# Performance work log

Measured on AMD Instinct MI355X. Metric: run time of the kernel, lower is better.

The kernel has to match this reference:

```python
import jax, jax.numpy as jnp
import numpy as np
from jax import lax
from itertools import combinations

# ---- static MiniRocket config (mirrors MiniRocketFeatures defaults) ----
NUM_KERNELS = 84
KSIZE = 9
C_IN = 9
SEQ_LEN = 2048
BATCH = 64
NUM_FEATURES = 10000
MAX_DIL_PER_KERNEL = 32

def _set_dilations(input_length):
    nfpk = NUM_FEATURES // NUM_KERNELS          # 119 features per kernel
    tmd = min(nfpk, MAX_DIL_PER_KERNEL)         # 32
    multiplier = nfpk / tmd
    max_exponent = np.log2((input_length - 1) / (KSIZE - 1))
    dilations, counts = np.unique(
        np.logspace(0, max_exponent, tmd, base=2).astype(np.int32),
        return_counts=True)
    nfd = (counts * multiplier).astype(np.int32)
    remainder = nfpk - nfd.sum()
    i = 0
    while remainder > 0:
        nfd[i] += 1; remainder -= 1; i = (i + 1) % len(nfd)
    return [int(d) for d in dilations], [int(n) for n in nfd]

DILATIONS, NFD = _set_dilations(SEQ_LEN)
NUM_DIL = len(DILATIONS)
PADDINGS = [(KSIZE - 1) * d // 2 for d in DILATIONS]
MAX_NF = max(NFD)


def _make_kernels():
    # 84 fixed ternary kernels: -1 everywhere, 2 at each 3-of-9 combination
    idx = np.array(list(combinations(range(KSIZE), 3)))       # [84, 3]
    k = -np.ones((NUM_KERNELS, KSIZE), np.float32)
    k[np.arange(NUM_KERNELS)[:, None], idx] = 2.0
    # grouped conv weight: repeat the 84-kernel block per input channel
    return np.tile(k, (C_IN, 1)).reshape(C_IN * NUM_KERNELS, 1, KSIZE)


def setup_inputs() -> dict:
    key = jax.random.key(0)
    k1, k2, k3 = jax.random.split(key, 3)
    x = jax.random.normal(k1, (BATCH, C_IN, SEQ_LEN), dtype=jnp.float32)
    kernels = jnp.asarray(_make_kernels())                    # [c_in*84, 1, 9]
    # per-dilation 0/1 channel-combination masks (1, c_in, 84, 1) stacked
    channel_combinations = jax.random.bernoulli(
        k2, 0.5, (NUM_DIL, C_IN, NUM_KERNELS)).astype(jnp.float32)
    # per-dilation biases [84, nf_i], padded to MAX_NF for stacking
    biases = jax.random.normal(
        k3, (NUM_DIL, NUM_KERNELS, MAX_NF), dtype=jnp.float32)
    return {"x": x, "kernels": kernels,
            "channel_combinations": channel_combinations, "biases": biases}


def _ppv(C, bias):
    # C: [B, K, T], bias: [K, nf] -> proportion of values above bias, [B, K*nf]
    ppv = (C[..., None] > bias[None, :, None, :]).astype(jnp.float32).mean(2)
    return ppv.reshape(C.shape[0], -1)


def reference(x, kernels, channel_combinations, biases):
    B = x.shape[0]
    feats = []
    for i, (dilation, padding) in enumerate(zip(DILATIONS, PADDINGS)):
        pad1 = i % 2
        # grouped dilated conv: [B, c_in*84, L] (output length == L since p = 4d)
        C = lax.conv_general_dilated(
            x, kernels, window_strides=(1,), padding=[(padding, padding)],
            rhs_dilation=(dilation,), feature_group_count=C_IN,
            dimension_numbers=("NCH", "OIH", "NCH"))
        C = C.reshape(B, C_IN, NUM_KERNELS, -1)
        # channel combine: multiply by 0/1 mask, sum over channels -> [B, 84, L]
        C = (C * channel_combinations[i][None, :, :, None]).sum(1)
        bias = biases[i][:, :NFD[i]]                          # [84, nf_i]
        # even-index kernels use full (padded) output
        feats.append(_ppv(C[:, pad1::2], bias[pad1::2]))
        # odd-index kernels use the valid (un-padded) region
        feats.append(_ppv(C[:, 1 - pad1::2, padding:-padding],
                          bias[1 - pad1::2]))
    return jnp.concatenate(feats, axis=1)                     # [B, 9996]
```

## Files before the change

### kernel.cpp

```cpp
#include <hip/hip_runtime.h>

#define NKER 84
#define NCH 9
#define SEQ 2048
#define NBATCH 64
#define NDIL 26
#define NFTOT 9996
#define MAXNF 15
#define NSLOT 28
#define NXCD 8

static constexpr int DILS[NDIL]   = {1,2,3,4,5,7,8,10,12,14,17,20,25,29,35,42,51,61,73,87,104,125,149,178,213,255};
static constexpr int NFDS[NDIL]   = {15,12,4,4,8,4,4,4,4,4,4,4,4,4,4,4,4,4,3,3,3,3,3,3,3,3};
static constexpr int CBASES[NDIL] = {0,1260,2268,2604,2940,3612,3948,4284,4620,4956,5292,5628,5964,6300,6636,6972,7308,7644,7980,8232,8484,8736,8988,9240,9492,9744};

typedef float f32x2u __attribute__((ext_vector_type(2), aligned(4)));

__device__ __forceinline__ float uniform_f(float v) {
    return __builtin_bit_cast(float, __builtin_amdgcn_readfirstlane(__builtin_bit_cast(int, v)));
}

__device__ __forceinline__ f32x2u pk_add(f32x2u a, f32x2u b) {
    f32x2u d;
    asm("v_pk_add_f32 %0, %1, %2" : "=v"(d) : "v"(a), "v"(b));
    return d;
}

template <int I>
__device__ __forceinline__ void body(const float* __restrict__ kw,
                                     const float* __restrict__ cc,
                                     const float* __restrict__ bias,
                                     float* __restrict__ out,
                                     const float* __restrict__ xb,
                                     float* __restrict__ y,
                                     int* __restrict__ cbuf,
                                     int b, int slot, int lane, int wv) {
    constexpr int D = DILS[I];
    constexpr int NF = NFDS[I];
    constexpr int P = 4 * D;
    constexpr int PAD1 = I & 1;
    constexpr int CBASE = CBASES[I];
    constexpr int RANGE = SEQ - 2 * P;
    constexpr int JLO = (P + 63) / 64;
    constexpr int JHI = (SEQ - P - 64) / 64;
    constexpr int NI  = (JHI + 1 > JLO) ? (JHI + 1 - JLO) : 0;
    constexpr int NI2 = NI / 2;
    constexpr bool IBR = (NI & 1) != 0;
    constexpr int JT0 = (JHI + 1 > JLO) ? (JHI + 1) : JLO;
    constexpr int MV2 = RANGE / 128;
    constexpr int TV1 = (RANGE - MV2 * 128) / 64;
    constexpr int REM = RANGE - MV2 * 128 - TV1 * 64;

    const float4* __restrict__ xb4 = (const float4*)xb;

    for (int k = slot; k < NKER; k += NSLOT) {
        __syncthreads();

        int mb = 0;
        for (int c = 0; c < NCH; ++c)
            if (cc[(I * NCH + c) * NKER + k] != 0.0f) mb |= (1 << c);
        mb = __builtin_amdgcn_readfirstlane(mb);

        int j0 = -1, j1 = -1, j2 = -1, no = 0;
        for (int j = 0; j < 9; ++j) {
            if (kw[k * 9 + j] > 0.0f) {
                if (no == 0) j0 = j; else if (no == 1) j1 = j; else j2 = j;
                ++no;
            }
        }
        j0 = __builtin_amdgcn_readfirstlane(j0);
        j1 = __builtin_amdgcn_readfirstlane(j1);
        j2 = __builtin_amdgcn_readfirstlane(j2);

        float w[9];
#pragma unroll
        for (int jj = 0; jj < 9; ++jj)
            w[jj] = uniform_f((jj == j0 || jj == j1 || jj == j2) ? 2.0f : -1.0f);

        float bs[NF];
#pragma unroll
        for (int f = 0; f < NF; ++f)
            bs[f] = uniform_f(bias[(I * NKER + k) * MAXNF + f]);

        {
            const int h = wv;
            f32x2u acc2[2 * (SEQ / 512)];
#pragma unroll
            for (int it = 0; it < 2 * (SEQ / 512); ++it)
                acc2[it] = (f32x2u){0.f, 0.f};
#pragma unroll
            for (int c = 0; c < NCH; ++c) {
                if (mb & (1 << c)) {
#pragma unroll
                    for (int it = 0; it < SEQ / 512; ++it) {
                        float4 v = xb4[c * (SEQ / 4) + h * (SEQ / 8) + it * 64 + lane];
                        acc2[2 * it]     = pk_add(acc2[2 * it],     (f32x2u){v.x, v.y});
                        acc2[2 * it + 1] = pk_add(acc2[2 * it + 1], (f32x2u){v.z, v.w});
                    }
                }
            }
#pragma unroll
            for (int it = 0; it < SEQ / 512; ++it)
                ((float4*)y)[h * (SEQ / 8) + it * 64 + lane] =
                    make_float4(acc2[2 * it].x, acc2[2 * it].y,
                                acc2[2 * it + 1].x, acc2[2 * it + 1].y);
        }
        __syncthreads();

        int cnt[NF];
#pragma unroll
        for (int f = 0; f < NF; ++f) cnt[f] = 0;

#define MRF_ITER2(TB) { \
            const int e0_ = (TB) + 2 * lane - 4 * D; \
            float CvA = 0.0f, CvB = 0.0f; \
            _Pragma("unroll") \
            for (int jj = 0; jj < 9; ++jj) { \
                f32x2u p_ = *(const f32x2u*)(y + e0_ + jj * D); \
                CvA = __builtin_fmaf(w[jj], p_.x, CvA); \
                CvB = __builtin_fmaf(w[jj], p_.y, CvB); \
            } \
            _Pragma("unroll") \
            for (int f = 0; f < NF; ++f) \
                cnt[f] += __popcll(__ballot(CvA > bs[f])) + __popcll(__ballot(CvB > bs[f])); }

#define MRF_ITER(TB) { \
            const int t_ = (TB) + lane; \
            float Cv = 0.0f; \
            _Pragma("unroll") \
            for (int jj = 0; jj < 9; ++jj) \
                Cv = __builtin_fmaf(w[jj], y[t_ + (jj - 4) * D], Cv); \
            _Pragma("unroll") \
            for (int f = 0; f < NF; ++f) \
                cnt[f] += __popcll(__ballot(Cv > bs[f])); }

#define MRF_MASKED(TB) { \
            const int t_ = (TB) + lane; \
            float Cv = 0.0f; \
            _Pragma("unroll") \
            for (int jj = 0; jj < 9; ++jj) { \
                const int lo_ = (TB) + (jj - 4) * D; \
                if (lo_ >= 0 && lo_ + 63 < SEQ) { \
                    Cv = __builtin_fmaf(w[jj], y[t_ + (jj - 4) * D], Cv); \
                } else if (lo_ + 63 >= 0 && lo_ < SEQ) { \
                    const int u_ = t_ + (jj - 4) * D; \
                    float v_ = y[u_ & (SEQ - 1)]; \
                    v_ = ((unsigned)u_ < (unsigned)SEQ) ? v_ : 0.0f; \
                    Cv = __builtin_fmaf(w[jj], v_, Cv); \
                } \
            } \
            _Pragma("unroll") \
            for (int f = 0; f < NF; ++f) \
                cnt[f] += __popcll(__ballot(Cv > bs[f])); }

        if ((k & 1) == PAD1) {
#pragma unroll
            for (int j = 0; j < JLO; ++j)
                if (((j >> 1) & 1) == wv) MRF_MASKED(j * 64)
#pragma unroll 2
            for (int a = wv; a < NI2; a += 2) MRF_ITER2(JLO * 64 + a * 128)
            if constexpr (IBR)
                if ((NI2 & 1) == wv) MRF_ITER(JLO * 64 + NI2 * 128)
#pragma unroll
            for (int j = JT0; j < SEQ / 64; ++j)
                if (((j >> 1) & 1) == wv) MRF_MASKED(j * 64)
        } else {
#pragma unroll 2
            for (int a = wv; a < MV2; a += 2) MRF_ITER2(P + a * 128)
            if constexpr (TV1)
                if ((MV2 & 1) == wv) MRF_ITER(P + MV2 * 128)
            if constexpr (REM != 0) {
                if (((MV2 + TV1) & 1) == wv) {
                    const int t = P + MV2 * 128 + TV1 * 64 + lane;
                    const int tr = (t < SEQ - P) ? t : (SEQ - P - 1);
                    const float* __restrict__ pb = y + tr - 4 * D;
                    float Cv = 0.0f;
#pragma unroll
                    for (int jj = 0; jj < 9; ++jj)
                        Cv = __builtin_fmaf(w[jj], pb[jj * D], Cv);
                    Cv = (t < SEQ - P) ? Cv : -3.402823466e38f;
#pragma unroll
                    for (int f = 0; f < NF; ++f)
                        cnt[f] += __popcll(__ballot(Cv > bs[f]));
                }
            }
        }

#undef MRF_ITER2
#undef MRF_ITER
#undef MRF_MASKED

        if (wv == 1 && lane == 0) {
#pragma unroll
            for (int f = 0; f < NF; ++f) cbuf[f] = cnt[f];
        }
        __syncthreads();
        if (wv == 0 && lane == 0) {
            const bool full = ((k & 1) == PAD1);
            const float invT = full ? (1.0f / (float)SEQ) : (1.0f / (float)RANGE);
            const int pos = full ? ((k - PAD1) >> 1) : (42 + ((k - (1 - PAD1)) >> 1));
            const int colb = CBASE + pos * NF;
#pragma unroll
            for (int f = 0; f < NF; ++f)
                out[(size_t)b * NFTOT + colb + f] = (float)(cnt[f] + cbuf[f]) * invT;
        }
    }
}

extern "C" __global__ void __launch_bounds__(128)
__attribute__((amdgpu_num_vgpr(128)))
mrf_kernel(const float* __restrict__ x, const float* __restrict__ kw,
           const float* __restrict__ cc, const float* __restrict__ bias,
           float* __restrict__ out) {
    __shared__ __align__(16) float ybuf[SEQ];
    __shared__ int cbuf[MAXNF];

    constexpr int NGRID = NDIL * NBATCH * NSLOT;
    constexpr int CHUNK = NGRID / NXCD;
    const int blk = (blockIdx.x % NXCD) * CHUNK + blockIdx.x / NXCD;

    const int s = blk % NSLOT;
    const int rest = blk / NSLOT;
    const int i = rest % NDIL;
    const int b = rest / NDIL;
    const int lane = threadIdx.x & 63;
    const int wv = __builtin_amdgcn_readfirstlane((int)(threadIdx.x >> 6));

    const float* xb = x + (size_t)b * (NCH * SEQ);

    switch (i) {
#define MRF_CASE(I) case I: body<I>(kw, cc, bias, out, xb, ybuf, cbuf, b, s, lane, wv); break;
        MRF_CASE(0)  MRF_CASE(1)  MRF_CASE(2)  MRF_CASE(3)  MRF_CASE(4)
        MRF_CASE(5)  MRF_CASE(6)  MRF_CASE(7)  MRF_CASE(8)  MRF_CASE(9)
        MRF_CASE(10) MRF_CASE(11) MRF_CASE(12) MRF_CASE(13) MRF_CASE(14)
        MRF_CASE(15) MRF_CASE(16) MRF_CASE(17) MRF_CASE(18) MRF_CASE(19)
        MRF_CASE(20) MRF_CASE(21) MRF_CASE(22) MRF_CASE(23) MRF_CASE(24)
        MRF_CASE(25)
#undef MRF_CASE
    }
}

extern "C" void kernel_launch(void* const* d_in, const int* in_sizes, int n_in,
                              void* d_out, int out_size, void* d_ws, size_t ws_size,
                              hipStream_t stream) {
    (void)in_sizes; (void)n_in; (void)d_ws; (void)ws_size; (void)out_size;
    const float* x    = (const float*)d_in[0];
    const float* kw   = (const float*)d_in[1];
    const float* cc   = (const float*)d_in[2];
    const float* bias = (const float*)d_in[3];
    float* out = (float*)d_out;

    mrf_kernel<<<dim3(NDIL * NBATCH * NSLOT), dim3(128), 0, stream>>>(x, kw, cc, bias, out);
}
```

Baseline: 316.9 us.

## Double-buffer the channel-combined LDS row and defer output writes across kernels

```diff
diff --git a/kernel.cpp b/kernel.cpp
--- a/kernel.cpp
+++ b/kernel.cpp
@@ -9,6 +9,8 @@
 #define MAXNF 15
 #define NSLOT 28
 #define NXCD 8
+#define WPB 2
+#define NK 3
 
 static constexpr int DILS[NDIL]   = {1,2,3,4,5,7,8,10,12,14,17,20,25,29,35,42,51,61,73,87,104,125,149,178,213,255};
 static constexpr int NFDS[NDIL]   = {15,12,4,4,8,4,4,4,4,4,4,4,4,4,4,4,4,4,3,3,3,3,3,3,3,3};
@@ -32,8 +34,8 @@
                                      const float* __restrict__ bias,
                                      float* __restrict__ out,
                                      const float* __restrict__ xb,
-                                     float* __restrict__ y,
-                                     int* __restrict__ cbuf,
+                                     float (* __restrict__ ybuf)[SEQ],
+                                     int (* __restrict__ cbuf)[WPB][MAXNF],
                                      int b, int slot, int lane, int wv) {
     constexpr int D = DILS[I];
     constexpr int NF = NFDS[I];
@@ -53,13 +55,54 @@
 
     const float4* __restrict__ xb4 = (const float4*)xb;
 
-    for (int k = slot; k < NKER; k += NSLOT) {
-        __syncthreads();
-
-        int mb = 0;
-        for (int c = 0; c < NCH; ++c)
-            if (cc[(I * NCH + c) * NKER + k] != 0.0f) mb |= (1 << c);
-        mb = __builtin_amdgcn_readfirstlane(mb);
+#define MRF_MB(K, DST) { \
+        int mb_ = 0; \
+        for (int c = 0; c < NCH; ++c) \
+            if (cc[(I * NCH + c) * NKER + (K)] != 0.0f) mb_ |= (1 << c); \
+        DST = __builtin_amdgcn_readfirstlane(mb_); }
+
+#define MRF_BUILD(DST, MB) { \
+        f32x2u acc2[2 * (SEQ / 512)]; \
+        _Pragma("unroll") \
+        for (int it2 = 0; it2 < 2 * (SEQ / 512); ++it2) \
+            acc2[it2] = (f32x2u){0.f, 0.f}; \
+        _Pragma("unroll") \
+        for (int c = 0; c < NCH; ++c) { \
+            if ((MB) & (1 << c)) { \
+                _Pragma("unroll") \
+                for (int it2 = 0; it2 < SEQ / 512; ++it2) { \
+                    float4 v = xb4[c * (SEQ / 4) + wv * (SEQ / 8) + it2 * 64 + lane]; \
+                    acc2[2 * it2]     = pk_add(acc2[2 * it2],     (f32x2u){v.x, v.y}); \
+                    acc2[2 * it2 + 1] = pk_add(acc2[2 * it2 + 1], (f32x2u){v.z, v.w}); \
+                } \
+            } \
+        } \
+        _Pragma("unroll") \
+        for (int it2 = 0; it2 < SEQ / 512; ++it2) \
+            ((float4*)(DST))[wv * (SEQ / 8) + it2 * 64 + lane] = \
+                make_float4(acc2[2 * it2].x, acc2[2 * it2].y, \
+                            acc2[2 * it2 + 1].x, acc2[2 * it2 + 1].y); }
+
+    int mb_cur;
+    MRF_MB(slot, mb_cur)
+    MRF_BUILD(ybuf[0], mb_cur)
+    __syncthreads();
+
+    for (int it = 0; it < NK; ++it) {
+        const int k = slot + it * NSLOT;
+        const float* __restrict__ y = ybuf[it & 1];
+
+        if (it > 0 && wv == 0 && lane == 0) {
+            const int kp = k - NSLOT;
+            const bool fullp = ((kp & 1) == PAD1);
+            const float invTp = fullp ? (1.0f / (float)SEQ) : (1.0f / (float)RANGE);
+            const int posp = fullp ? ((kp - PAD1) >> 1) : (42 + ((kp - (1 - PAD1)) >> 1));
+            const int colbp = CBASE + posp * NF;
+#pragma unroll
+            for (int f = 0; f < NF; ++f)
+                out[(size_t)b * NFTOT + colbp + f] =
+                    (float)(cbuf[it - 1][0][f] + cbuf[it - 1][1][f]) * invTp;
+        }
 
         int j0 = -1, j1 = -1, j2 = -1, no = 0;
         for (int j = 0; j < 9; ++j) {
@@ -81,31 +124,6 @@
 #pragma unroll
         for (int f = 0; f < NF; ++f)
             bs[f] = uniform_f(bias[(I * NKER + k) * MAXNF + f]);
-
-        {
-            const int h = wv;
-            f32x2u acc2[2 * (SEQ / 512)];
-#pragma unroll
-            for (int it = 0; it < 2 * (SEQ / 512); ++it)
-                acc2[it] = (f32x2u){0.f, 0.f};
-#pragma unroll
-            for (int c = 0; c < NCH; ++c) {
-                if (mb & (1 << c)) {
-#pragma unroll
-                    for (int it = 0; it < SEQ / 512; ++it) {
-                        float4 v = xb4[c * (SEQ / 4) + h * (SEQ / 8) + it * 64 + lane];
-                        acc2[2 * it]     = pk_add(acc2[2 * it],     (f32x2u){v.x, v.y});
-                        acc2[2 * it + 1] = pk_add(acc2[2 * it + 1], (f32x2u){v.z, v.w});
-                    }
-                }
-            }
-#pragma unroll
-            for (int it = 0; it < SEQ / 512; ++it)
-                ((float4*)y)[h * (SEQ / 8) + it * 64 + lane] =
-                    make_float4(acc2[2 * it].x, acc2[2 * it].y,
-                                acc2[2 * it + 1].x, acc2[2 * it + 1].y);
-        }
-        __syncthreads();
 
         int cnt[NF];
 #pragma unroll
@@ -190,30 +208,43 @@
 #undef MRF_ITER
 #undef MRF_MASKED
 
-        if (wv == 1 && lane == 0) {
-#pragma unroll
-            for (int f = 0; f < NF; ++f) cbuf[f] = cnt[f];
-        }
+        if (lane == 0) {
+#pragma unroll
+            for (int f = 0; f < NF; ++f) cbuf[it][wv][f] = cnt[f];
+        }
+
+        if (it + 1 < NK) {
+            int mbn;
+            MRF_MB(k + NSLOT, mbn)
+            MRF_BUILD(ybuf[(it + 1) & 1], mbn)
+        }
+
         __syncthreads();
-        if (wv == 0 && lane == 0) {
-            const bool full = ((k & 1) == PAD1);
-            const float invT = full ? (1.0f / (float)SEQ) : (1.0f / (float)RANGE);
-            const int pos = full ? ((k - PAD1) >> 1) : (42 + ((k - (1 - PAD1)) >> 1));
-            const int colb = CBASE + pos * NF;
-#pragma unroll
-            for (int f = 0; f < NF; ++f)
-                out[(size_t)b * NFTOT + colb + f] = (float)(cnt[f] + cbuf[f]) * invT;
-        }
     }
-}
-
-extern "C" __global__ void __launch_bounds__(128)
+
+    if (wv == 0 && lane == 0) {
+        const int kl = slot + (NK - 1) * NSLOT;
+        const bool fulll = ((kl & 1) == PAD1);
+        const float invTl = fulll ? (1.0f / (float)SEQ) : (1.0f / (float)RANGE);
+        const int posl = fulll ? ((kl - PAD1) >> 1) : (42 + ((kl - (1 - PAD1)) >> 1));
+        const int colbl = CBASE + posl * NF;
+#pragma unroll
+        for (int f = 0; f < NF; ++f)
+            out[(size_t)b * NFTOT + colbl + f] =
+                (float)(cbuf[NK - 1][0][f] + cbuf[NK - 1][1][f]) * invTl;
+    }
+
+#undef MRF_MB
+#undef MRF_BUILD
+}
+
+extern "C" __global__ void __launch_bounds__(WPB * 64)
 __attribute__((amdgpu_num_vgpr(128)))
 mrf_kernel(const float* __restrict__ x, const float* __restrict__ kw,
            const float* __restrict__ cc, const float* __restrict__ bias,
            float* __restrict__ out) {
-    __shared__ __align__(16) float ybuf[SEQ];
-    __shared__ int cbuf[MAXNF];
+    __shared__ __align__(16) float ybuf[2][SEQ];
+    __shared__ int cbuf[NK][WPB][MAXNF];
 
     constexpr int NGRID = NDIL * NBATCH * NSLOT;
     constexpr int CHUNK = NGRID / NXCD;
@@ -250,5 +281,5 @@
     const float* bias = (const float*)d_in[3];
     float* out = (float*)d_out;
 
-    mrf_kernel<<<dim3(NDIL * NBATCH * NSLOT), dim3(128), 0, stream>>>(x, kw, cc, bias, out);
-}
+    mrf_kernel<<<dim3(NDIL * NBATCH * NSLOT), dim3(WPB * 64), 0, stream>>>(x, kw, cc, bias, out);
+}
```

Result: slower. 331.4 us (+4.6%).

## Process kernel pairs per iteration, sharing x loads for channel-combine

Applied to the files above, without the earlier changes.

```diff
diff --git a/kernel.cpp b/kernel.cpp
--- a/kernel.cpp
+++ b/kernel.cpp
@@ -7,8 +7,10 @@
 #define NDIL 26
 #define NFTOT 9996
 #define MAXNF 15
-#define NSLOT 28
+#define NSLOT 14
 #define NXCD 8
+#define WPB 2
+#define NPAIR 3
 
 static constexpr int DILS[NDIL]   = {1,2,3,4,5,7,8,10,12,14,17,20,25,29,35,42,51,61,73,87,104,125,149,178,213,255};
 static constexpr int NFDS[NDIL]   = {15,12,4,4,8,4,4,4,4,4,4,4,4,4,4,4,4,4,3,3,3,3,3,3,3,3};
@@ -32,8 +34,8 @@
                                      const float* __restrict__ bias,
                                      float* __restrict__ out,
                                      const float* __restrict__ xb,
-                                     float* __restrict__ y,
-                                     int* __restrict__ cbuf,
+                                     float (* __restrict__ ybuf)[SEQ],
+                                     int (* __restrict__ cbuf)[WPB][MAXNF],
                                      int b, int slot, int lane, int wv) {
     constexpr int D = DILS[I];
     constexpr int NF = NFDS[I];
@@ -53,167 +55,185 @@
 
     const float4* __restrict__ xb4 = (const float4*)xb;
 
-    for (int k = slot; k < NKER; k += NSLOT) {
+#define MRF_MB(K, DST) { \
+        int mb_ = 0; \
+        for (int c = 0; c < NCH; ++c) \
+            if (cc[(I * NCH + c) * NKER + (K)] != 0.0f) mb_ |= (1 << c); \
+        DST = __builtin_amdgcn_readfirstlane(mb_); }
+
+    for (int g = 0; g < NPAIR; ++g) {
+        const int k0 = slot + g * (2 * NSLOT);
+
         __syncthreads();
 
-        int mb = 0;
-        for (int c = 0; c < NCH; ++c)
-            if (cc[(I * NCH + c) * NKER + k] != 0.0f) mb |= (1 << c);
-        mb = __builtin_amdgcn_readfirstlane(mb);
-
-        int j0 = -1, j1 = -1, j2 = -1, no = 0;
-        for (int j = 0; j < 9; ++j) {
-            if (kw[k * 9 + j] > 0.0f) {
-                if (no == 0) j0 = j; else if (no == 1) j1 = j; else j2 = j;
-                ++no;
-            }
-        }
-        j0 = __builtin_amdgcn_readfirstlane(j0);
-        j1 = __builtin_amdgcn_readfirstlane(j1);
-        j2 = __builtin_amdgcn_readfirstlane(j2);
-
-        float w[9];
-#pragma unroll
-        for (int jj = 0; jj < 9; ++jj)
-            w[jj] = uniform_f((jj == j0 || jj == j1 || jj == j2) ? 2.0f : -1.0f);
-
-        float bs[NF];
-#pragma unroll
-        for (int f = 0; f < NF; ++f)
-            bs[f] = uniform_f(bias[(I * NKER + k) * MAXNF + f]);
-
-        {
-            const int h = wv;
-            f32x2u acc2[2 * (SEQ / 512)];
-#pragma unroll
-            for (int it = 0; it < 2 * (SEQ / 512); ++it)
-                acc2[it] = (f32x2u){0.f, 0.f};
+        int mb0, mb1;
+        MRF_MB(k0, mb0)
+        MRF_MB(k0 + NSLOT, mb1)
+
+#pragma unroll
+        for (int it = 0; it < SEQ / 512; ++it) {
+            f32x2u a0l = {0.f, 0.f}, a0h = {0.f, 0.f};
+            f32x2u a1l = {0.f, 0.f}, a1h = {0.f, 0.f};
 #pragma unroll
             for (int c = 0; c < NCH; ++c) {
-                if (mb & (1 << c)) {
-#pragma unroll
-                    for (int it = 0; it < SEQ / 512; ++it) {
-                        float4 v = xb4[c * (SEQ / 4) + h * (SEQ / 8) + it * 64 + lane];
-                        acc2[2 * it]     = pk_add(acc2[2 * it],     (f32x2u){v.x, v.y});
-                        acc2[2 * it + 1] = pk_add(acc2[2 * it + 1], (f32x2u){v.z, v.w});
+                if ((mb0 | mb1) & (1 << c)) {
+                    float4 v = xb4[c * (SEQ / 4) + wv * (SEQ / 8) + it * 64 + lane];
+                    if (mb0 & (1 << c)) {
+                        a0l = pk_add(a0l, (f32x2u){v.x, v.y});
+                        a0h = pk_add(a0h, (f32x2u){v.z, v.w});
+                    }
+                    if (mb1 & (1 << c)) {
+                        a1l = pk_add(a1l, (f32x2u){v.x, v.y});
+                        a1h = pk_add(a1h, (f32x2u){v.z, v.w});
                     }
                 }
             }
-#pragma unroll
-            for (int it = 0; it < SEQ / 512; ++it)
-                ((float4*)y)[h * (SEQ / 8) + it * 64 + lane] =
-                    make_float4(acc2[2 * it].x, acc2[2 * it].y,
-                                acc2[2 * it + 1].x, acc2[2 * it + 1].y);
+            ((float4*)ybuf[0])[wv * (SEQ / 8) + it * 64 + lane] =
+                make_float4(a0l.x, a0l.y, a0h.x, a0h.y);
+            ((float4*)ybuf[1])[wv * (SEQ / 8) + it * 64 + lane] =
+                make_float4(a1l.x, a1l.y, a1h.x, a1h.y);
         }
         __syncthreads();
 
-        int cnt[NF];
-#pragma unroll
-        for (int f = 0; f < NF; ++f) cnt[f] = 0;
+        for (int kk = 0; kk < 2; ++kk) {
+            const int k = k0 + kk * NSLOT;
+            const float* __restrict__ y = ybuf[kk];
+
+            int j0 = -1, j1 = -1, j2 = -1, no = 0;
+            for (int j = 0; j < 9; ++j) {
+                if (kw[k * 9 + j] > 0.0f) {
+                    if (no == 0) j0 = j; else if (no == 1) j1 = j; else j2 = j;
+                    ++no;
+                }
+            }
+            j0 = __builtin_amdgcn_readfirstlane(j0);
+            j1 = __builtin_amdgcn_readfirstlane(j1);
+            j2 = __builtin_amdgcn_readfirstlane(j2);
+
+            float w[9];
+#pragma unroll
+            for (int jj = 0; jj < 9; ++jj)
+                w[jj] = uniform_f((jj == j0 || jj == j1 || jj == j2) ? 2.0f : -1.0f);
+
+            float bs[NF];
+#pragma unroll
+            for (int f = 0; f < NF; ++f)
+                bs[f] = uniform_f(bias[(I * NKER + k) * MAXNF + f]);
+
+            int cnt[NF];
+#pragma unroll
+            for (int f = 0; f < NF; ++f) cnt[f] = 0;
 
 #define MRF_ITER2(TB) { \
-            const int e0_ = (TB) + 2 * lane - 4 * D; \
-            float CvA = 0.0f, CvB = 0.0f; \
-            _Pragma("unroll") \
-            for (int jj = 0; jj < 9; ++jj) { \
-                f32x2u p_ = *(const f32x2u*)(y + e0_ + jj * D); \
-                CvA = __builtin_fmaf(w[jj], p_.x, CvA); \
-                CvB = __builtin_fmaf(w[jj], p_.y, CvB); \
-            } \
-            _Pragma("unroll") \
-            for (int f = 0; f < NF; ++f) \
-                cnt[f] += __popcll(__ballot(CvA > bs[f])) + __popcll(__ballot(CvB > bs[f])); }
+                const int e0_ = (TB) + 2 * lane - 4 * D; \
+                float CvA = 0.0f, CvB = 0.0f; \
+                _Pragma("unroll") \
+                for (int jj = 0; jj < 9; ++jj) { \
+                    f32x2u p_ = *(const f32x2u*)(y + e0_ + jj * D); \
+                    CvA = __builtin_fmaf(w[jj], p_.x, CvA); \
+                    CvB = __builtin_fmaf(w[jj], p_.y, CvB); \
+                } \
+                _Pragma("unroll") \
+                for (int f = 0; f < NF; ++f) \
+                    cnt[f] += __popcll(__ballot(CvA > bs[f])) + __popcll(__ballot(CvB > bs[f])); }
 
 #define MRF_ITER(TB) { \
-            const int t_ = (TB) + lane; \
-            float Cv = 0.0f; \
-            _Pragma("unroll") \
-            for (int jj = 0; jj < 9; ++jj) \
-                Cv = __builtin_fmaf(w[jj], y[t_ + (jj - 4) * D], Cv); \
-            _Pragma("unroll") \
-            for (int f = 0; f < NF; ++f) \
-                cnt[f] += __popcll(__ballot(Cv > bs[f])); }
+                const int t_ = (TB) + lane; \
+                float Cv = 0.0f; \
+                _Pragma("unroll") \
+                for (int jj = 0; jj < 9; ++jj) \
+                    Cv = __builtin_fmaf(w[jj], y[t_ + (jj - 4) * D], Cv); \
+                _Pragma("unroll") \
+                for (int f = 0; f < NF; ++f) \
+                    cnt[f] += __popcll(__ballot(Cv > bs[f])); }
 
 #define MRF_MASKED(TB) { \
-            const int t_ = (TB) + lane; \
-            float Cv = 0.0f; \
-            _Pragma("unroll") \
-            for (int jj = 0; jj < 9; ++jj) { \
-                const int lo_ = (TB) + (jj - 4) * D; \
-                if (lo_ >= 0 && lo_ + 63 < SEQ) { \
-                    Cv = __builtin_fmaf(w[jj], y[t_ + (jj - 4) * D], Cv); \
-                } else if (lo_ + 63 >= 0 && lo_ < SEQ) { \
-                    const int u_ = t_ + (jj - 4) * D; \
-                    float v_ = y[u_ & (SEQ - 1)]; \
-                    v_ = ((unsigned)u_ < (unsigned)SEQ) ? v_ : 0.0f; \
-                    Cv = __builtin_fmaf(w[jj], v_, Cv); \
+                const int t_ = (TB) + lane; \
+                float Cv = 0.0f; \
+                _Pragma("unroll") \
+                for (int jj = 0; jj < 9; ++jj) { \
+                    const int lo_ = (TB) + (jj - 4) * D; \
+                    if (lo_ >= 0 && lo_ + 63 < SEQ) { \
+                        Cv = __builtin_fmaf(w[jj], y[t_ + (jj - 4) * D], Cv); \
+                    } else if (lo_ + 63 >= 0 && lo_ < SEQ) { \
+                        const int u_ = t_ + (jj - 4) * D; \
+                        float v_ = y[u_ & (SEQ - 1)]; \
+                        v_ = ((unsigned)u_ < (unsigned)SEQ) ? v_ : 0.0f; \
+                        Cv = __builtin_fmaf(w[jj], v_, Cv); \
+                    } \
                 } \
-            } \
-            _Pragma("unroll") \
-            for (int f = 0; f < NF; ++f) \
-                cnt[f] += __popcll(__ballot(Cv > bs[f])); }
-
-        if ((k & 1) == PAD1) {
-#pragma unroll
-            for (int j = 0; j < JLO; ++j)
-                if (((j >> 1) & 1) == wv) MRF_MASKED(j * 64)
+                _Pragma("unroll") \
+                for (int f = 0; f < NF; ++f) \
+                    cnt[f] += __popcll(__ballot(Cv > bs[f])); }
+
+            if ((k & 1) == PAD1) {
+#pragma unroll
+                for (int j = 0; j < JLO; ++j)
+                    if (((j >> 1) & 1) == wv) MRF_MASKED(j * 64)
 #pragma unroll 2
-            for (int a = wv; a < NI2; a += 2) MRF_ITER2(JLO * 64 + a * 128)
-            if constexpr (IBR)
-                if ((NI2 & 1) == wv) MRF_ITER(JLO * 64 + NI2 * 128)
-#pragma unroll
-            for (int j = JT0; j < SEQ / 64; ++j)
-                if (((j >> 1) & 1) == wv) MRF_MASKED(j * 64)
-        } else {
+                for (int a = wv; a < NI2; a += 2) MRF_ITER2(JLO * 64 + a * 128)
+                if constexpr (IBR)
+                    if ((NI2 & 1) == wv) MRF_ITER(JLO * 64 + NI2 * 128)
+#pragma unroll
+                for (int j = JT0; j < SEQ / 64; ++j)
+                    if (((j >> 1) & 1) == wv) MRF_MASKED(j * 64)
+            } else {
 #pragma unroll 2
-            for (int a = wv; a < MV2; a += 2) MRF_ITER2(P + a * 128)
-            if constexpr (TV1)
-                if ((MV2 & 1) == wv) MRF_ITER(P + MV2 * 128)
-            if constexpr (REM != 0) {
-                if (((MV2 + TV1) & 1) == wv) {
-                    const int t = P + MV2 * 128 + TV1 * 64 + lane;
-                    const int tr = (t < SEQ - P) ? t : (SEQ - P - 1);
-                    const float* __restrict__ pb = y + tr - 4 * D;
-                    float Cv = 0.0f;
-#pragma unroll
-                    for (int jj = 0; jj < 9; ++jj)
-                        Cv = __builtin_fmaf(w[jj], pb[jj * D], Cv);
-                    Cv = (t < SEQ - P) ? Cv : -3.402823466e38f;
-#pragma unroll
-                    for (int f = 0; f < NF; ++f)
-                        cnt[f] += __popcll(__ballot(Cv > bs[f]));
+                for (int a = wv; a < MV2; a += 2) MRF_ITER2(P + a * 128)
+                if constexpr (TV1)
+                    if ((MV2 & 1) == wv) MRF_ITER(P + MV2 * 128)
+                if constexpr (REM != 0) {
+                    if (((MV2 + TV1) & 1) == wv) {
+                        const int t = P + MV2 * 128 + TV1 * 64 + lane;
+                        const int tr = (t < SEQ - P) ? t : (SEQ - P - 1);
+                        const float* __restrict__ pb = y + tr - 4 * D;
+                        float Cv = 0.0f;
+#pragma unroll
+                        for (int jj = 0; jj < 9; ++jj)
+                            Cv = __builtin_fmaf(w[jj], pb[jj * D], Cv);
+                        Cv = (t < SEQ - P) ? Cv : -3.402823466e38f;
+#pragma unroll
+                        for (int f = 0; f < NF; ++f)
+                            cnt[f] += __popcll(__ballot(Cv > bs[f]));
+                    }
                 }
             }
-        }
 
 #undef MRF_ITER2
 #undef MRF_ITER
 #undef MRF_MASKED
 
-        if (wv == 1 && lane == 0) {
-#pragma unroll
-            for (int f = 0; f < NF; ++f) cbuf[f] = cnt[f];
+            if (lane == 0) {
+#pragma unroll
+                for (int f = 0; f < NF; ++f) cbuf[kk][wv][f] = cnt[f];
+            }
         }
+
         __syncthreads();
-        if (wv == 0 && lane == 0) {
+
+        if (lane == 0) {
+            const int k = k0 + wv * NSLOT;
             const bool full = ((k & 1) == PAD1);
             const float invT = full ? (1.0f / (float)SEQ) : (1.0f / (float)RANGE);
             const int pos = full ? ((k - PAD1) >> 1) : (42 + ((k - (1 - PAD1)) >> 1));
             const int colb = CBASE + pos * NF;
 #pragma unroll
             for (int f = 0; f < NF; ++f)
-                out[(size_t)b * NFTOT + colb + f] = (float)(cnt[f] + cbuf[f]) * invT;
+                out[(size_t)b * NFTOT + colb + f] =
+                    (float)(cbuf[wv][0][f] + cbuf[wv][1][f]) * invT;
         }
     }
-}
-
-extern "C" __global__ void __launch_bounds__(128)
+
+#undef MRF_MB
+}
+
+extern "C" __global__ void __launch_bounds__(WPB * 64)
 __attribute__((amdgpu_num_vgpr(128)))
 mrf_kernel(const float* __restrict__ x, const float* __restrict__ kw,
            const float* __restrict__ cc, const float* __restrict__ bias,
            float* __restrict__ out) {
-    __shared__ __align__(16) float ybuf[SEQ];
-    __shared__ int cbuf[MAXNF];
+    __shared__ __align__(16) float ybuf[2][SEQ];
+    __shared__ int cbuf[2][WPB][MAXNF];
 
     constexpr int NGRID = NDIL * NBATCH * NSLOT;
     constexpr int CHUNK = NGRID / NXCD;
@@ -250,5 +270,5 @@
     const float* bias = (const float*)d_in[3];
     float* out = (float*)d_out;
 
-    mrf_kernel<<<dim3(NDIL * NBATCH * NSLOT), dim3(128), 0, stream>>>(x, kw, cc, bias, out);
-}
+    mrf_kernel<<<dim3(NDIL * NBATCH * NSLOT), dim3(WPB * 64), 0, stream>>>(x, kw, cc, bias, out);
+}
```

After: 381.7 us. 1.2x slower.
